# Kernel optimization log

Measured on AMD Instinct MI355X. Metric: run time of the kernel, lower is better.

## Reference

```python
import jax, jax.numpy as jnp
import numpy as np

BN_EPS = 1e-5
N_EULER = 8


def _bn_train(x, gamma, beta):
    # BatchNorm1d in training mode: biased batch statistics over the batch axis
    mu = jnp.mean(x, axis=0)
    var = jnp.mean((x - mu) ** 2, axis=0)
    return gamma * (x - mu) / jnp.sqrt(var + BN_EPS) + beta


def setup_inputs() -> dict:
    key = jax.random.key(0)
    ks = jax.random.split(key, 16)
    B, d, u_dim, n_obs, sdim = 4096, 512, 64, 25, 128
    h1, h2, hd = 1024, 1024, 512

    def w(k, shape, fan_in):
        return jax.random.normal(k, shape, dtype=jnp.float32) / np.sqrt(fan_in)

    return {
        "z_dyn": jax.random.normal(ks[0], (B, d), dtype=jnp.float32),
        "z_static": jax.random.normal(ks[1], (B, sdim), dtype=jnp.float32),
        "dt": jnp.array(0.05, dtype=jnp.float32),
        "ut": jax.random.normal(ks[2], (B, u_dim), dtype=jnp.float32),
        "eps": jax.random.normal(ks[3], (N_EULER, B, d), dtype=jnp.float32),
        "W1": w(ks[4], (h1, d), d), "b1": jnp.zeros((h1,), jnp.float32),
        "g1": jnp.ones((h1,), jnp.float32), "be1": jnp.zeros((h1,), jnp.float32),
        "W2": w(ks[5], (h2, h1), h1), "b2": jnp.zeros((h2,), jnp.float32),
        "g2": jnp.ones((h2,), jnp.float32), "be2": jnp.zeros((h2,), jnp.float32),
        "W3": w(ks[6], (d, h2), h2), "b3": jnp.zeros((d,), jnp.float32),
        "Wd1": w(ks[7], (hd, d), d), "bd1": jnp.zeros((hd,), jnp.float32),
        "Wd2": w(ks[8], (d, hd), hd), "bd2": jnp.zeros((d,), jnp.float32),
        "B_sde": w(ks[9], (d, u_dim), u_dim),
        "C": w(ks[10], (n_obs, d), d),
        "D": w(ks[11], (n_obs, u_dim), u_dim),
    }


def reference(z_dyn, z_static, dt, ut, eps,
              W1, b1, g1, be1, W2, b2, g2, be2, W3, b3,
              Wd1, bd1, Wd2, bd2, B_sde, C, D):
    h = dt / N_EULER
    sqrt_h = jnp.sqrt(jnp.abs(h) + 1e-8)

    def drift(z):
        a = jax.nn.relu(_bn_train(z @ W1.T + b1, g1, be1))
        a = jax.nn.relu(_bn_train(a @ W2.T + b2, g2, be2))
        return a @ W3.T + b3

    def diffusion(z):
        t = jnp.tanh(z @ Wd1.T + bd1)
        return jax.nn.softplus(t @ Wd2.T + bd2) + 1e-5

    def step(z, e):
        f = drift(z)
        g = diffusion(z)
        z = z + h * f + sqrt_h * g * e  # Euler-Maruyama update (training mode)
        return z, None

    z, _ = jax.lax.scan(step, z_dyn, eps)
    ut_dt = ut * dt
    z_next = z + ut_dt @ B_sde.T
    yt = z_next @ C.T + ut_dt @ D.T
    return (z_next, yt)
```

## Files before the change

### kernel.cpp

```cpp
#include <hip/hip_runtime.h>


typedef unsigned short ushort_t;
typedef __bf16 bf16x8 __attribute__((ext_vector_type(8)));
typedef float f32x4 __attribute__((ext_vector_type(4)));

__device__ __forceinline__ float bf2f(ushort_t s) {
  unsigned u = ((unsigned)s) << 16;
  return __uint_as_float(u);
}
__device__ __forceinline__ ushort_t f2bf(float f) {
  unsigned u = __float_as_uint(f);
  unsigned lsb = (u >> 16) & 1u;
  u += 0x7fffu + lsb;
  return (ushort_t)(u >> 16);
}
__device__ __forceinline__ float ldin(const void* p, size_t i, int f32) {
  return f32 ? ((const float*)p)[i] : bf2f(((const ushort_t*)p)[i]);
}
__device__ __forceinline__ void async16(const void* g, void* l) {
  __builtin_amdgcn_global_load_lds(
      (const __attribute__((address_space(1))) void*)g,
      (__attribute__((address_space(3))) void*)l, 16, 0, 0);
}

template <int N>
__device__ __forceinline__ void waitvm() {
  if constexpr (N == 0) {
    asm volatile("s_waitcnt vmcnt(0)" ::: "memory");
  } else if constexpr (N == 4) {
    asm volatile("s_waitcnt vmcnt(4)" ::: "memory");
  } else if constexpr (N == 6) {
    asm volatile("s_waitcnt vmcnt(6)" ::: "memory");
  }
  __builtin_amdgcn_sched_barrier(0);
}
__device__ __forceinline__ void waitlgkm0() {
  asm volatile("s_waitcnt lgkmcnt(0)" ::: "memory");
  __builtin_amdgcn_sched_barrier(0);
}

__device__ __forceinline__ bf16x8 lds_frag(const __bf16* T, int row, int kb) {
  const int byte = (row << 7) + ((((kb >> 3) ^ (row & 7))) << 4);
  return *(const bf16x8*)((const char*)T + byte);
}

__global__ void k_detect(const void* __restrict__ eps, const void* __restrict__ dtraw,
                         float* __restrict__ consts) {
  __shared__ float mx[256];
  const int t = threadIdx.x;
  const ushort_t* e = (const ushort_t*)eps;
  float m = 0.f;
#pragma unroll
  for (int k = 0; k < 4; ++k) {
    float v = fabsf(bf2f(e[t * 4 + k]));
    if (!(v < 1e30f)) v = 1e30f;
    m = fmaxf(m, v);
  }
  mx[t] = m;
  __syncthreads();
  if (t == 0) {
    float M = 0.f;
    for (int k = 0; k < 256; ++k) M = fmaxf(M, mx[k]);
    const int f32 = (M > 1e3f) ? 1 : 0;
    float dt;
    if (f32) {
      dt = *(const float*)dtraw;
    } else {
      float db = bf2f(*(const ushort_t*)dtraw);
      float df = *(const float*)dtraw;
      dt = (db > 1e-6f && db < 1e3f) ? db : df;
    }
    const float h = dt * 0.125f;
    consts[0] = h;
    consts[1] = sqrtf(fabsf(h) + 1e-8f);
    consts[2] = dt;
    consts[3] = (float)f32;
  }
}

struct ConvArgs { const void* src[5]; };
#define CONV_TOT 2621440

__global__ void k_conv(ConvArgs a, const float* __restrict__ consts,
                       ushort_t* __restrict__ base) {
  constexpr int CUM[6] = {0, 524288, 786432, 1835008, 2359296, 2621440};
  const int f32 = consts[3] != 0.f;
  const int i = (blockIdx.x * 256 + threadIdx.x) * 4;
  if (i >= CONV_TOT) return;
  int j = 0;
#pragma unroll
  for (int k = 1; k < 5; ++k)
    if (i >= CUM[k]) j = k;
  const int local = i - CUM[j];
  const void* s = a.src[j];
  ushort4 o;
  if (f32) {
    float4 v = ((const float4*)s)[local >> 2];
    o = make_ushort4(f2bf(v.x), f2bf(v.y), f2bf(v.z), f2bf(v.w));
  } else {
    o = ((const ushort4*)s)[local >> 2];
  }
  *(ushort4*)(base + i) = o;
}

template <int MT, int MODE, int STATS, int FUSE, int BIAS, int FINAL, int ANORM>
__device__ __forceinline__ void gemm_body(
    const ushort_t* __restrict__ A, const ushort_t* __restrict__ W,
    const void* __restrict__ bias, int ncol0, ushort_t* __restrict__ Cout,
    int Nout, int K, int m0, int n0, __bf16* As, __bf16* Bs,
    float* __restrict__ s1, float* __restrict__ s2,
    const ushort_t* __restrict__ Gb, float* __restrict__ zf,
    ushort_t* __restrict__ zb, const void* __restrict__ eps,
    unsigned long long eoff, const float* __restrict__ consts,
    const float* __restrict__ Ub, float* __restrict__ out0,
    const float* __restrict__ s1in, const float* __restrict__ s2in,
    const void* __restrict__ gsc, const void* __restrict__ gbe,
    float* scF, float* shF, float* sS) {
  constexpr int BM = MT * 64;
  constexpr int LPT = MT * 2 + 2;
  const int f32 = consts[3] != 0.f;
  const int tid = threadIdx.x;
  const int lane = tid & 63;
  const int wave = tid >> 6;
  const int col = lane & 15;
  const int quad = lane >> 4;
  const int rowBase = wave * (MT * 16);

  const int srow = tid >> 3;
  const int skc = tid & 7;
  auto stageA = [&](int k0, __bf16* dst) {
#pragma unroll
    for (int j = 0; j < BM / 32; ++j) {
      const int row = j * 32 + srow;
      async16(A + (size_t)(m0 + row) * K + k0 + (((skc ^ (row & 7))) << 3),
              (char*)dst + (j * 256 + tid) * 16);
    }
  };
  auto stageB = [&](int k0, __bf16* dst) {
#pragma unroll
    for (int j = 0; j < 2; ++j) {
      const int row = j * 32 + srow;
      async16(W + (size_t)(n0 + row) * K + k0 + (((skc ^ (row & 7))) << 3),
              (char*)dst + (j * 256 + tid) * 16);
    }
  };

  f32x4 acc[MT][4] = {};

  __bf16* Acur = As;
  __bf16* Aalt = As + BM * 64;
  __bf16* Bcur = Bs;
  __bf16* Balt = Bs + 64 * 64;

  stageA(0, Acur);
  stageB(0, Bcur);

  if (ANORM) {
    const float inv = 1.0f / 4096.0f;
    for (int c = tid; c < K; c += 256) {
      float mu = s1in[c] * inv;
      float var = fmaxf(s2in[c] * inv - mu * mu, 0.f);
      float sc = ldin(gsc, c, f32) * rsqrtf(var + 1e-5f);
      scF[c] = sc;
      shF[c] = ldin(gbe, c, f32) - mu * sc;
    }
  }
  waitlgkm0();
  __builtin_amdgcn_s_barrier();

  const int NIT = K / 64;
  for (int it = 0; it < NIT; ++it) {
    const int k0 = it * 64;
    if (it + 1 < NIT) {
      stageA(k0 + 64, Aalt);
      stageB(k0 + 64, Balt);
      waitvm<LPT>();
    } else {
      waitvm<0>();
    }
    __builtin_amdgcn_s_barrier();

#pragma unroll
    for (int kk = 0; kk < 2; ++kk) {
      const int kb = kk * 32 + quad * 8;
      bf16x8 af[MT], bfr[4];
      if (ANORM) {
        float sc8[8], sh8[8];
        *(float4*)&sc8[0] = *(const float4*)&scF[k0 + kb];
        *(float4*)&sc8[4] = *(const float4*)&scF[k0 + kb + 4];
        *(float4*)&sh8[0] = *(const float4*)&shF[k0 + kb];
        *(float4*)&sh8[4] = *(const float4*)&shF[k0 + kb + 4];
#pragma unroll
        for (int mt = 0; mt < MT; ++mt) {
          bf16x8 raw = lds_frag(Acur, rowBase + mt * 16 + col, kb);
#pragma unroll
          for (int j = 0; j < 8; ++j)
            af[mt][j] =
                (__bf16)fmaxf(fmaf((float)raw[j], sc8[j], sh8[j]), 0.f);
        }
      } else {
#pragma unroll
        for (int mt = 0; mt < MT; ++mt)
          af[mt] = lds_frag(Acur, rowBase + mt * 16 + col, kb);
      }
#pragma unroll
      for (int nt = 0; nt < 4; ++nt)
        bfr[nt] = lds_frag(Bcur, nt * 16 + col, kb);
      __builtin_amdgcn_s_setprio(1);
#pragma unroll
      for (int mt = 0; mt < MT; ++mt)
#pragma unroll
        for (int nt = 0; nt < 4; ++nt)
          acc[mt][nt] = __builtin_amdgcn_mfma_f32_16x16x32_bf16(
              af[mt], bfr[nt], acc[mt][nt], 0, 0, 0);
      __builtin_amdgcn_s_setprio(0);
    }
    waitlgkm0();
    __builtin_amdgcn_s_barrier();
    __bf16* t0 = Acur; Acur = Aalt; Aalt = t0;
    __bf16* t1 = Bcur; Bcur = Balt; Balt = t1;
  }

  if (STATS) {
    for (int i = tid; i < 128; i += 256) sS[i] = 0.f;
    __syncthreads();
  }

  const float h = consts[0], sh = consts[1];

#pragma unroll
  for (int nt = 0; nt < 4; ++nt) {
    const int gn = n0 + nt * 16 + col;
    const float bv = BIAS ? ldin(bias, gn + ncol0, f32) : 0.f;
    float ls = 0.f, lq = 0.f;
#pragma unroll
    for (int mt = 0; mt < MT; ++mt) {
#pragma unroll
      for (int r = 0; r < 4; ++r) {
        const int gm = m0 + rowBase + mt * 16 + quad * 4 + r;
        float v = acc[mt][nt][r] + bv;
        if (STATS) {
          ls += v;
          lq += v * v;
        }
        if (MODE == 1) {
          v = tanhf(v);
        } else if (MODE == 2) {
          v = fmaxf(v, 0.f) + log1pf(expf(-fabsf(v))) + 1e-5f;
        }
        const size_t o = (size_t)gm * Nout + gn + ncol0;
        if (FUSE) {
          const float e = ldin(eps, eoff + o, f32);
          const float g = bf2f(Gb[o]);
          const float z = zf[o] + h * v + sh * g * e;
          zf[o] = z;
          zb[o] = f2bf(z);
          if (FINAL) out0[o] = z + Ub[o];
        } else {
          Cout[o] = f2bf(v);
        }
      }
    }
    if (STATS) {
      atomicAdd(&sS[nt * 16 + col], ls);
      atomicAdd(&sS[64 + nt * 16 + col], lq);
    }
  }

  if (STATS) {
    __syncthreads();
    if (tid < 64) {
      atomicAdd(&s1[n0 + tid], sS[tid]);
      atomicAdd(&s2[n0 + tid], sS[64 + tid]);
    }
  }
}

__global__ __launch_bounds__(256, 3) void k_x1t(
    const ushort_t* __restrict__ zb, const ushort_t* __restrict__ Wcat,
    const void* __restrict__ bd1, ushort_t* __restrict__ Xb,
    ushort_t* __restrict__ Tb, float* __restrict__ s1, float* __restrict__ s2,
    const float* __restrict__ consts) {
  __shared__ __bf16 As[2 * 128 * 64] __attribute__((aligned(16)));
  __shared__ __bf16 Bs[2 * 64 * 64] __attribute__((aligned(16)));
  __shared__ float sS[128];
  const int L = blockIdx.x;
  const int q = L & 7, w = L >> 3;
  const int mloc = w & 3, n = w >> 2;
  const int m0 = (q * 4 + mloc) * 128;
  const int n0 = n * 64;
  if (n < 16) {
    gemm_body<2, 0, 1, 0, 0, 0, 0>(
        zb, Wcat, nullptr, 0, Xb, 1024, 512, m0, n0, As, Bs, s1, s2, nullptr,
        nullptr, nullptr, nullptr, 0, consts, nullptr, nullptr, nullptr,
        nullptr, nullptr, nullptr, nullptr, nullptr, sS);
  } else {
    gemm_body<2, 1, 0, 0, 1, 0, 0>(
        zb, Wcat, bd1, -1024, Tb, 512, 512, m0, n0, As, Bs, nullptr, nullptr,
        nullptr, nullptr, nullptr, nullptr, 0, consts, nullptr, nullptr,
        nullptr, nullptr, nullptr, nullptr, nullptr, nullptr, sS);
  }
}

__global__ __launch_bounds__(256, 2) void k_x2g(
    const ushort_t* __restrict__ X1raw, const ushort_t* __restrict__ W2c,
    const ushort_t* __restrict__ Tb, const ushort_t* __restrict__ Wd2c,
    const void* __restrict__ bd2, ushort_t* __restrict__ Ab,
    ushort_t* __restrict__ Gb, float* __restrict__ s1o, float* __restrict__ s2o,
    const float* __restrict__ s1i, const float* __restrict__ s2i,
    const void* __restrict__ g1, const void* __restrict__ be1,
    const float* __restrict__ consts) {
  __shared__ __bf16 As[2 * 128 * 64] __attribute__((aligned(16)));
  __shared__ __bf16 Bs[2 * 64 * 64] __attribute__((aligned(16)));
  __shared__ float scF[1024], shF[1024];
  __shared__ float sS[128];
  const int L = blockIdx.x;
  if (L < 512) {
    const int q = L & 7, w = L >> 3;
    const int mloc = w & 3, n = w >> 2;
    const int m0 = (q * 4 + mloc) * 128, n0 = n * 64;
    gemm_body<2, 0, 1, 0, 0, 0, 1>(
        X1raw, W2c, nullptr, 0, Ab, 1024, 1024, m0, n0, As, Bs, s1o, s2o,
        nullptr, nullptr, nullptr, nullptr, 0, consts, nullptr, nullptr, s1i,
        s2i, g1, be1, scF, shF, sS);
  } else {
    const int Lg = L - 512;
    const int q = Lg & 7, w = Lg >> 3;
    const int mloc = w & 7, n = w >> 3;
    const int m0 = (q * 8 + mloc) * 64, n0 = n * 64;
    gemm_body<1, 2, 0, 0, 1, 0, 0>(
        Tb, Wd2c, bd2, 0, Gb, 512, 512, m0, n0, As, Bs, nullptr, nullptr,
        nullptr, nullptr, nullptr, nullptr, 0, consts, nullptr, nullptr,
        nullptr, nullptr, nullptr, nullptr, nullptr, nullptr, sS);
  }
}

template <int FINAL>
__global__ __launch_bounds__(256, 4) void k_fupd(
    const ushort_t* __restrict__ X2raw, const ushort_t* __restrict__ W3c,
    const void* __restrict__ b3, const ushort_t* __restrict__ Gb,
    float* __restrict__ zf, ushort_t* __restrict__ zb,
    const void* __restrict__ eps, unsigned long long eoff,
    const float* __restrict__ consts, const float* __restrict__ Ub,
    float* __restrict__ out0, const float* __restrict__ s1i,
    const float* __restrict__ s2i, const void* __restrict__ g2,
    const void* __restrict__ be2) {
  __shared__ __bf16 As[2 * 64 * 64] __attribute__((aligned(16)));
  __shared__ __bf16 Bs[2 * 64 * 64] __attribute__((aligned(16)));
  __shared__ float scF[1024], shF[1024];
  const int L = blockIdx.x;
  const int q = L & 7, w = L >> 3;
  const int mloc = w & 7, n = w >> 3;
  const int m0 = (q * 8 + mloc) * 64, n0 = n * 64;
  gemm_body<1, 0, 0, 1, 1, FINAL, 1>(
      X2raw, W3c, b3, 0, nullptr, 512, 1024, m0, n0, As, Bs, nullptr, nullptr,
      Gb, zf, zb, eps, eoff, consts, Ub, out0, s1i, s2i, g2, be2, scF, shF,
      nullptr);
}

__global__ void k_init(const void* __restrict__ z, float* __restrict__ zf,
                       ushort_t* __restrict__ zb, const float* __restrict__ consts) {
  const int f32 = consts[3] != 0.f;
  const int i = blockIdx.x * 256 + threadIdx.x;
  float4 v;
  if (f32) {
    v = ((const float4*)z)[i];
  } else {
    ushort4 u = ((const ushort4*)z)[i];
    v = make_float4(bf2f(u.x), bf2f(u.y), bf2f(u.z), bf2f(u.w));
  }
  ((float4*)zf)[i] = v;
  ((ushort4*)zb)[i] = make_ushort4(f2bf(v.x), f2bf(v.y), f2bf(v.z), f2bf(v.w));
}

__global__ __launch_bounds__(256) void k_ub(
    const void* __restrict__ ut, const void* __restrict__ Bsde,
    const float* __restrict__ consts, float* __restrict__ Ub) {
  __shared__ float As[64][68];
  __shared__ float Bs[64][68];
  const float dt = consts[2];
  const int f32 = consts[3] != 0.f;
  const int t = threadIdx.x;
  const int tx = t & 15, ty = t >> 4;
  const int n0 = blockIdx.x * 64, m0 = blockIdx.y * 64;
  const int r = t >> 2;
  const int c0 = (t & 3) * 16;

#pragma unroll
  for (int j = 0; j < 16; ++j) {
    As[c0 + j][r] = ldin(ut, (size_t)(m0 + r) * 64 + c0 + j, f32);
    Bs[c0 + j][r] = ldin(Bsde, (size_t)(n0 + r) * 64 + c0 + j, f32);
  }
  __syncthreads();

  float acc[4][4] = {};
#pragma unroll 8
  for (int kk = 0; kk < 64; ++kk) {
    float a[4], b[4];
    *(float4*)a = *(const float4*)&As[kk][ty * 4];
    *(float4*)b = *(const float4*)&Bs[kk][tx * 4];
#pragma unroll
    for (int i = 0; i < 4; ++i)
#pragma unroll
      for (int j = 0; j < 4; ++j) acc[i][j] += a[i] * b[j];
  }

#pragma unroll
  for (int i = 0; i < 4; ++i) {
    const size_t o = (size_t)(m0 + ty * 4 + i) * 512 + n0 + tx * 4;
    *(float4*)&Ub[o] = make_float4(dt * acc[i][0], dt * acc[i][1],
                                   dt * acc[i][2], dt * acc[i][3]);
  }
}

__global__ void k_deff(const void* __restrict__ Cm, const void* __restrict__ Bsde,
                       const void* __restrict__ Dm, const float* __restrict__ consts,
                       float* __restrict__ Deff) {
  __shared__ float red[4][64];
  const int f32 = consts[3] != 0.f;
  const int j = blockIdx.x;
  const int k = threadIdx.x & 63;
  const int part = threadIdx.x >> 6;
  float acc = 0.f;
  const int l0 = part * 128;
#pragma unroll 8
  for (int l = l0; l < l0 + 128; ++l)
    acc += ldin(Cm, (size_t)j * 512 + l, f32) * ldin(Bsde, (size_t)l * 64 + k, f32);
  red[part][k] = acc;
  __syncthreads();
  if (part == 0) {
    float s = red[0][k] + red[1][k] + red[2][k] + red[3][k];
    Deff[j * 64 + k] = s + ldin(Dm, (size_t)j * 64 + k, f32);
  }
}

__global__ __launch_bounds__(256) void k_final2(
    const float* __restrict__ zf, const void* __restrict__ ut,
    const float* __restrict__ consts, const void* __restrict__ Cm,
    const float* __restrict__ Deff, float* __restrict__ out1) {
  const float dt = consts[2];
  const int f32 = consts[3] != 0.f;
  const int t = threadIdx.x;
  const int lane = t & 63;
  const int m = blockIdx.x * 4 + (t >> 6);
  float z8[8];
#pragma unroll
  for (int i = 0; i < 8; ++i) z8[i] = zf[(size_t)m * 512 + i * 64 + lane];
  const float u = ldin(ut, (size_t)m * 64 + lane, f32);

  for (int j = 0; j < 25; ++j) {
    float p = dt * u * Deff[j * 64 + lane];
#pragma unroll
    for (int i = 0; i < 8; ++i)
      p += z8[i] * ldin(Cm, (size_t)j * 512 + i * 64 + lane, f32);
#pragma unroll
    for (int off = 32; off > 0; off >>= 1) p += __shfl_down(p, off, 64);
    if (lane == 0) out1[m * 25 + j] = p;
  }
}

extern "C" void kernel_launch(void* const* d_in, const int* in_sizes, int n_in,
                              void* d_out, int out_size, void* d_ws, size_t ws_size,
                              hipStream_t stream) {
  static const int expA[22] = {
      2097152, 524288, 1,      262144, 16777216, 524288, 1024, 1024,
      1024,    1048576, 1024,  1024,   1024,     524288, 512,  262144,
      512,     262144, 512,    32768,  12800,    1600};

  int map[21];
  bool okA = (n_in == 22), okB = (n_in == 21);
  if (okA)
    for (int i = 0; i < 22; ++i)
      if (in_sizes[i] != expA[i]) { okA = false; break; }
  if (okB) {
    int j = 0;
    for (int i = 0; i < 22; ++i) {
      if (i == 1) continue;
      if (in_sizes[j] != expA[i]) { okB = false; break; }
      ++j;
    }
  }
  if (okA) {
    map[0] = 0;
    for (int i = 1; i < 21; ++i) map[i] = i + 1;
  } else if (okB) {
    for (int i = 0; i < 21; ++i) map[i] = i;
  } else {
    map[0] = 0;
    for (int i = 1; i < 21; ++i) map[i] = (i + 1 < n_in) ? i + 1 : n_in - 1;
  }

  const void* z_dyn = d_in[map[0]];
  const void* dtp = d_in[map[1]];
  const void* ut = d_in[map[2]];
  const void* eps = d_in[map[3]];
  const void* W1 = d_in[map[4]];
  const void* g1 = d_in[map[6]];
  const void* be1 = d_in[map[7]];
  const void* W2 = d_in[map[8]];
  const void* g2 = d_in[map[10]];
  const void* be2 = d_in[map[11]];
  const void* W3 = d_in[map[12]];
  const void* b3 = d_in[map[13]];
  const void* Wd1 = d_in[map[14]];
  const void* bd1 = d_in[map[15]];
  const void* Wd2 = d_in[map[16]];
  const void* bd2 = d_in[map[17]];
  const void* Bsde = d_in[map[18]];
  const void* Cm = d_in[map[19]];
  const void* Dm = d_in[map[20]];

  char* ws = (char*)d_ws;
  const size_t MB = 1024 * 1024;
  float* zf = (float*)(ws + 0);
  ushort_t* zb = (ushort_t*)(ws + 8 * MB);
  ushort_t* Xb = (ushort_t*)(ws + 12 * MB);
  ushort_t* Ab = (ushort_t*)(ws + 20 * MB);
  ushort_t* Tb = (ushort_t*)(ws + 28 * MB);
  ushort_t* Gb = (ushort_t*)(ws + 32 * MB);
  float* Ub = (float*)(ws + 36 * MB);
  ushort_t* canon = (ushort_t*)(ws + 44 * MB);
  float* stats = (float*)(ws + 49 * MB + 512 * 1024);
  float* consts = stats + 16 * 2048;
  float* Deff = consts + 16;

  const ushort_t* Wcat = canon + 0;
  const ushort_t* W2c = canon + 786432;
  const ushort_t* W3c = canon + 1835008;
  const ushort_t* Wd2c = canon + 2359296;

  float* out_z = (float*)d_out;
  float* out_y = out_z + 4096 * 512;

  const dim3 blk(256);

  k_detect<<<1, blk, 0, stream>>>(eps, dtp, consts);

  ConvArgs ca;
  ca.src[0] = W1;
  ca.src[1] = Wd1;
  ca.src[2] = W2;
  ca.src[3] = W3;
  ca.src[4] = Wd2;
  k_conv<<<(CONV_TOT / 4 + 255) / 256, blk, 0, stream>>>(ca, consts, canon);

  hipMemsetAsync(stats, 0, 16 * 2048 * sizeof(float), stream);
  k_init<<<2048, blk, 0, stream>>>(z_dyn, zf, zb, consts);
  k_ub<<<dim3(8, 64), blk, 0, stream>>>(ut, Bsde, consts, Ub);
  k_deff<<<25, blk, 0, stream>>>(Cm, Bsde, Dm, consts, Deff);

  for (int s = 0; s < 8; ++s) {
    float* sA1 = stats + (s * 2 + 0) * 2048;
    float* sA2 = stats + (s * 2 + 1) * 2048;
    const unsigned long long eoff = (unsigned long long)s * 4096 * 512;

    k_x1t<<<768, blk, 0, stream>>>(zb, Wcat, bd1, Xb, Tb,
                                   sA1, sA1 + 1024, consts);

    k_x2g<<<1024, blk, 0, stream>>>(Xb, W2c, Tb, Wd2c, bd2, Ab, Gb,
                                    sA2, sA2 + 1024, sA1, sA1 + 1024,
                                    g1, be1, consts);

    if (s < 7) {
      k_fupd<0><<<512, blk, 0, stream>>>(Ab, W3c, b3, Gb, zf, zb, eps, eoff,
                                         consts, Ub, out_z, sA2, sA2 + 1024,
                                         g2, be2);
    } else {
      k_fupd<1><<<512, blk, 0, stream>>>(Ab, W3c, b3, Gb, zf, zb, eps, eoff,
                                         consts, Ub, out_z, sA2, sA2 + 1024,
                                         g2, be2);
    }
  }

  k_final2<<<1024, blk, 0, stream>>>(zf, ut, consts, Cm, Deff, out_y);
}
```

Measured before the change: 830.1 us.

## Store BN scale/shift as fp16, compile-time K, rebalance diffusion GEMM tiles

The K dimension becomes a template parameter, so loop counts and strides are known at compile time. The BatchNorm scale and shift tables in LDS are stored as fp16 instead of fp32, which halves their shared-memory footprint and lets k_x2g request 3 blocks per CU instead of 2. The diffusion GEMM in k_x2g switches to 128-row tiles, cutting its block count and the grid from 1024 to 768 blocks. Keeping scale and shift in fp16 loses some precision in the normalization, and the larger tiles change the load balance.

Measured after the change: 766.9 us. -7.6%, faster.

```diff
diff --git a/kernel.cpp b/kernel.cpp
--- a/kernel.cpp
+++ b/kernel.cpp
@@ -3,6 +3,7 @@
 
 typedef unsigned short ushort_t;
 typedef __bf16 bf16x8 __attribute__((ext_vector_type(8)));
+typedef _Float16 f16x8 __attribute__((ext_vector_type(8)));
 typedef float f32x4 __attribute__((ext_vector_type(4)));
 
 __device__ __forceinline__ float bf2f(ushort_t s) {
@@ -104,11 +105,12 @@
   *(ushort4*)(base + i) = o;
 }
 
-template <int MT, int MODE, int STATS, int FUSE, int BIAS, int FINAL, int ANORM>
+template <int MT, int KT, int MODE, int STATS, int FUSE, int BIAS, int FINAL,
+          int ANORM>
 __device__ __forceinline__ void gemm_body(
     const ushort_t* __restrict__ A, const ushort_t* __restrict__ W,
     const void* __restrict__ bias, int ncol0, ushort_t* __restrict__ Cout,
-    int Nout, int K, int m0, int n0, __bf16* As, __bf16* Bs,
+    int Nout, int m0, int n0, __bf16* As, __bf16* Bs,
     float* __restrict__ s1, float* __restrict__ s2,
     const ushort_t* __restrict__ Gb, float* __restrict__ zf,
     ushort_t* __restrict__ zb, const void* __restrict__ eps,
@@ -116,7 +118,7 @@
     const float* __restrict__ Ub, float* __restrict__ out0,
     const float* __restrict__ s1in, const float* __restrict__ s2in,
     const void* __restrict__ gsc, const void* __restrict__ gbe,
-    float* scF, float* shF, float* sS) {
+    _Float16* scF, _Float16* shF, float* sS) {
   constexpr int BM = MT * 64;
   constexpr int LPT = MT * 2 + 2;
   const int f32 = consts[3] != 0.f;
@@ -133,7 +135,7 @@
 #pragma unroll
     for (int j = 0; j < BM / 32; ++j) {
       const int row = j * 32 + srow;
-      async16(A + (size_t)(m0 + row) * K + k0 + (((skc ^ (row & 7))) << 3),
+      async16(A + (size_t)(m0 + row) * KT + k0 + (((skc ^ (row & 7))) << 3),
               (char*)dst + (j * 256 + tid) * 16);
     }
   };
@@ -141,7 +143,7 @@
 #pragma unroll
     for (int j = 0; j < 2; ++j) {
       const int row = j * 32 + srow;
-      async16(W + (size_t)(n0 + row) * K + k0 + (((skc ^ (row & 7))) << 3),
+      async16(W + (size_t)(n0 + row) * KT + k0 + (((skc ^ (row & 7))) << 3),
               (char*)dst + (j * 256 + tid) * 16);
     }
   };
@@ -158,18 +160,21 @@
 
   if (ANORM) {
     const float inv = 1.0f / 4096.0f;
-    for (int c = tid; c < K; c += 256) {
+#pragma unroll
+    for (int c0 = 0; c0 < KT; c0 += 256) {
+      const int c = c0 + tid;
       float mu = s1in[c] * inv;
       float var = fmaxf(s2in[c] * inv - mu * mu, 0.f);
       float sc = ldin(gsc, c, f32) * rsqrtf(var + 1e-5f);
-      scF[c] = sc;
-      shF[c] = ldin(gbe, c, f32) - mu * sc;
+      scF[c] = (_Float16)sc;
+      shF[c] = (_Float16)(ldin(gbe, c, f32) - mu * sc);
     }
   }
   waitlgkm0();
   __builtin_amdgcn_s_barrier();
 
-  const int NIT = K / 64;
+  constexpr int NIT = KT / 64;
+#pragma unroll 1
   for (int it = 0; it < NIT; ++it) {
     const int k0 = it * 64;
     if (it + 1 < NIT) {
@@ -186,18 +191,15 @@
       const int kb = kk * 32 + quad * 8;
       bf16x8 af[MT], bfr[4];
       if (ANORM) {
-        float sc8[8], sh8[8];
-        *(float4*)&sc8[0] = *(const float4*)&scF[k0 + kb];
-        *(float4*)&sc8[4] = *(const float4*)&scF[k0 + kb + 4];
-        *(float4*)&sh8[0] = *(const float4*)&shF[k0 + kb];
-        *(float4*)&sh8[4] = *(const float4*)&shF[k0 + kb + 4];
+        f16x8 scv = *(const f16x8*)&scF[k0 + kb];
+        f16x8 shv = *(const f16x8*)&shF[k0 + kb];
 #pragma unroll
         for (int mt = 0; mt < MT; ++mt) {
           bf16x8 raw = lds_frag(Acur, rowBase + mt * 16 + col, kb);
 #pragma unroll
           for (int j = 0; j < 8; ++j)
-            af[mt][j] =
-                (__bf16)fmaxf(fmaf((float)raw[j], sc8[j], sh8[j]), 0.f);
+            af[mt][j] = (__bf16)fmaxf(
+                fmaf((float)raw[j], (float)scv[j], (float)shv[j]), 0.f);
         }
       } else {
 #pragma unroll
@@ -291,19 +293,19 @@
   const int m0 = (q * 4 + mloc) * 128;
   const int n0 = n * 64;
   if (n < 16) {
-    gemm_body<2, 0, 1, 0, 0, 0, 0>(
-        zb, Wcat, nullptr, 0, Xb, 1024, 512, m0, n0, As, Bs, s1, s2, nullptr,
+    gemm_body<2, 512, 0, 1, 0, 0, 0, 0>(
+        zb, Wcat, nullptr, 0, Xb, 1024, m0, n0, As, Bs, s1, s2, nullptr,
         nullptr, nullptr, nullptr, 0, consts, nullptr, nullptr, nullptr,
         nullptr, nullptr, nullptr, nullptr, nullptr, sS);
   } else {
-    gemm_body<2, 1, 0, 0, 1, 0, 0>(
-        zb, Wcat, bd1, -1024, Tb, 512, 512, m0, n0, As, Bs, nullptr, nullptr,
-        nullptr, nullptr, nullptr, nullptr, 0, consts, nullptr, nullptr,
-        nullptr, nullptr, nullptr, nullptr, nullptr, nullptr, sS);
-  }
-}
-
-__global__ __launch_bounds__(256, 2) void k_x2g(
+    gemm_body<2, 512, 1, 0, 0, 1, 0, 0>(
+        zb, Wcat, bd1, -1024, Tb, 512, m0, n0, As, Bs, nullptr,
+        nullptr, nullptr, nullptr, nullptr, nullptr, 0, consts, nullptr,
+        nullptr, nullptr, nullptr, nullptr, nullptr, nullptr, nullptr, sS);
+  }
+}
+
+__global__ __launch_bounds__(256, 3) void k_x2g(
     const ushort_t* __restrict__ X1raw, const ushort_t* __restrict__ W2c,
     const ushort_t* __restrict__ Tb, const ushort_t* __restrict__ Wd2c,
     const void* __restrict__ bd2, ushort_t* __restrict__ Ab,
@@ -313,24 +315,25 @@
     const float* __restrict__ consts) {
   __shared__ __bf16 As[2 * 128 * 64] __attribute__((aligned(16)));
   __shared__ __bf16 Bs[2 * 64 * 64] __attribute__((aligned(16)));
-  __shared__ float scF[1024], shF[1024];
+  __shared__ _Float16 scF[1024] __attribute__((aligned(16)));
+  __shared__ _Float16 shF[1024] __attribute__((aligned(16)));
   __shared__ float sS[128];
   const int L = blockIdx.x;
   if (L < 512) {
     const int q = L & 7, w = L >> 3;
     const int mloc = w & 3, n = w >> 2;
     const int m0 = (q * 4 + mloc) * 128, n0 = n * 64;
-    gemm_body<2, 0, 1, 0, 0, 0, 1>(
-        X1raw, W2c, nullptr, 0, Ab, 1024, 1024, m0, n0, As, Bs, s1o, s2o,
+    gemm_body<2, 1024, 0, 1, 0, 0, 0, 1>(
+        X1raw, W2c, nullptr, 0, Ab, 1024, m0, n0, As, Bs, s1o, s2o,
         nullptr, nullptr, nullptr, nullptr, 0, consts, nullptr, nullptr, s1i,
         s2i, g1, be1, scF, shF, sS);
   } else {
     const int Lg = L - 512;
     const int q = Lg & 7, w = Lg >> 3;
-    const int mloc = w & 7, n = w >> 3;
-    const int m0 = (q * 8 + mloc) * 64, n0 = n * 64;
-    gemm_body<1, 2, 0, 0, 1, 0, 0>(
-        Tb, Wd2c, bd2, 0, Gb, 512, 512, m0, n0, As, Bs, nullptr, nullptr,
+    const int mloc = w & 3, n = w >> 2;
+    const int m0 = (q * 4 + mloc) * 128, n0 = n * 64;
+    gemm_body<2, 512, 2, 0, 0, 1, 0, 0>(
+        Tb, Wd2c, bd2, 0, Gb, 512, m0, n0, As, Bs, nullptr, nullptr,
         nullptr, nullptr, nullptr, nullptr, 0, consts, nullptr, nullptr,
         nullptr, nullptr, nullptr, nullptr, nullptr, nullptr, sS);
   }
@@ -348,13 +351,14 @@
     const void* __restrict__ be2) {
   __shared__ __bf16 As[2 * 64 * 64] __attribute__((aligned(16)));
   __shared__ __bf16 Bs[2 * 64 * 64] __attribute__((aligned(16)));
-  __shared__ float scF[1024], shF[1024];
+  __shared__ _Float16 scF[1024] __attribute__((aligned(16)));
+  __shared__ _Float16 shF[1024] __attribute__((aligned(16)));
   const int L = blockIdx.x;
   const int q = L & 7, w = L >> 3;
   const int mloc = w & 7, n = w >> 3;
   const int m0 = (q * 8 + mloc) * 64, n0 = n * 64;
-  gemm_body<1, 0, 0, 1, 1, FINAL, 1>(
-      X2raw, W3c, b3, 0, nullptr, 512, 1024, m0, n0, As, Bs, nullptr, nullptr,
+  gemm_body<1, 1024, 0, 0, 1, 1, FINAL, 1>(
+      X2raw, W3c, b3, 0, nullptr, 512, m0, n0, As, Bs, nullptr, nullptr,
       Gb, zf, zb, eps, eoff, consts, Ub, out0, s1i, s2i, g2, be2, scF, shF,
       nullptr);
 }
@@ -558,9 +562,9 @@
     k_x1t<<<768, blk, 0, stream>>>(zb, Wcat, bd1, Xb, Tb,
                                    sA1, sA1 + 1024, consts);
 
-    k_x2g<<<1024, blk, 0, stream>>>(Xb, W2c, Tb, Wd2c, bd2, Ab, Gb,
-                                    sA2, sA2 + 1024, sA1, sA1 + 1024,
-                                    g1, be1, consts);
+    k_x2g<<<768, blk, 0, stream>>>(Xb, W2c, Tb, Wd2c, bd2, Ab, Gb,
+                                   sA2, sA2 + 1024, sA1, sA1 + 1024,
+                                   g1, be1, consts);
 
     if (s < 7) {
       k_fupd<0><<<512, blk, 0, stream>>>(Ab, W3c, b3, Gb, zf, zb, eps, eoff,
```
